# Kernel optimization log

Hardware: AMD Instinct MI355X
Metric: run time of the kernel (lower is better)

The kernel has to match this reference:

```python
import math
import jax, jax.numpy as jnp
import numpy as np

EMBED_SIZE = 1024
NUM_HEADS = 16
HEAD_DIM = EMBED_SIZE // NUM_HEADS
N, L = 8, 1024
MASK_FILL = -1e3  # value used by masked_fill in the original (NOT -inf)
SCALE = 1.0 / math.sqrt(EMBED_SIZE)  # original divides by embed_size**0.5, not head_dim


def setup_inputs() -> dict:
    key = jax.random.key(0)
    ks = jax.random.split(key, 7)
    values = jax.random.normal(ks[0], (N, L, EMBED_SIZE), dtype=jnp.float32)
    keys_t = jax.random.normal(ks[1], (N, L, EMBED_SIZE), dtype=jnp.float32)
    queries = jax.random.normal(ks[2], (N, L, EMBED_SIZE), dtype=jnp.float32)
    attn_mask = jax.random.randint(ks[3], (1, 1, L, L), 0, 2, dtype=jnp.int32)
    scr_key_padding_mask = jax.random.randint(ks[4], (N, 1, 1, L), 0, 2, dtype=jnp.int32)
    # fc_out: nn.Linear(embed_size, embed_size) with bias
    fc_w = jax.random.normal(ks[5], (EMBED_SIZE, EMBED_SIZE), dtype=jnp.float32) * (1.0 / math.sqrt(EMBED_SIZE))
    fc_b = jax.random.normal(ks[6], (EMBED_SIZE,), dtype=jnp.float32) * 0.01
    return {"values": values, "keys": keys_t, "queries": queries,
            "fc_w": fc_w, "fc_b": fc_b,
            "attn_mask": attn_mask, "scr_key_padding_mask": scr_key_padding_mask}


def reference(values, keys, queries, fc_w, fc_b, attn_mask, scr_key_padding_mask):
    n, q_len, e = queries.shape
    k_len = keys.shape[1]
    h, d = NUM_HEADS, HEAD_DIM
    # NOTE: the original defines per-head Linear projections but never applies them
    v = values.reshape(n, k_len, h, d)
    k = keys.reshape(n, k_len, h, d)
    q = queries.reshape(n, q_len, h, d)
    energy = jnp.einsum('nqhd,nkhd->nhqk', q, k)  # [n, h, q, k]
    am = attn_mask[:, :, :k_len, :k_len]
    energy = jnp.where(am == 0, MASK_FILL, energy)
    energy = jnp.where(scr_key_padding_mask == 0, MASK_FILL, energy)
    attention = jax.nn.softmax(energy * SCALE, axis=3)
    out = jnp.einsum('nhql,nlhd->nqhd', attention, v).reshape(n, q_len, h * d)
    return out @ fc_w.T + fc_b
```

## Files before the change

### kernel.cpp

```cpp
#include <hip/hip_runtime.h>

#define L_SEQ 1024
#define EMB 1024
#define NH 16
#define HD 64

typedef _Float16 half8 __attribute__((ext_vector_type(8)));
typedef _Float16 half4v __attribute__((ext_vector_type(4)));
typedef float f32x4 __attribute__((ext_vector_type(4)));
typedef float fvec4 __attribute__((ext_vector_type(4)));
typedef unsigned int u32;
typedef unsigned long long u64;

constexpr float C2 = 0.045084220027780106f;
constexpr float F2 = -45.08422002778011f;

constexpr int FP = 40;
constexpr int PP = 72;

__device__ __forceinline__ void async16(const void* g, void* l) {
    __builtin_amdgcn_global_load_lds((const __attribute__((address_space(1))) u32*)g,
                                     (__attribute__((address_space(3))) u32*)l, 16, 0, 0);
}

__global__ void pack_mask_kernel(const int* __restrict__ am, u32* __restrict__ bits) {
    const int i = blockIdx.x * 256 + threadIdx.x;
    const int lane = threadIdx.x & 63;
    u64 b = __ballot(am[i] != 0);
    if (lane == 0)       bits[i >> 5] = (u32)b;
    else if (lane == 32) bits[i >> 5] = (u32)(b >> 32);
}

__global__ void convert_w_kernel(const float* __restrict__ w, _Float16* __restrict__ o) {
    size_t i = ((size_t)blockIdx.x * blockDim.x + threadIdx.x) * 4;
    fvec4 v = *(const fvec4*)(w + i);
    half4v h;
#pragma unroll
    for (int j = 0; j < 4; ++j) h[j] = (_Float16)v[j];
    *(half4v*)(o + i) = h;
}

__global__ __launch_bounds__(256) void cvt_kv_kernel(
    const float* __restrict__ keys, const float* __restrict__ values,
    _Float16* __restrict__ K16, _Float16* __restrict__ Vt16)
{
    __shared__ __align__(16) _Float16 Vt[64 * PP];
    const int tid = threadIdx.x;
    const int kt = blockIdx.x, h = blockIdx.y, n = blockIdx.z;
    const int kbase = kt * 64;
    const int r = tid >> 2, c0 = (tid & 3) * 16;
    const int nh = n * NH + h;

    {
        const float* src = keys + ((size_t)(n * L_SEQ + kbase + r)) * EMB + h * HD + c0;
        fvec4 a0 = *(const fvec4*)(src),     a1 = *(const fvec4*)(src + 4);
        fvec4 a2 = *(const fvec4*)(src + 8), a3 = *(const fvec4*)(src + 12);
        half8 o0, o1;
#pragma unroll
        for (int j = 0; j < 4; ++j) {
            o0[j] = (_Float16)a0[j]; o0[j + 4] = (_Float16)a1[j];
            o1[j] = (_Float16)a2[j]; o1[j + 4] = (_Float16)a3[j];
        }
        _Float16* dst = K16 + ((size_t)nh * L_SEQ + kbase + r) * HD + c0;
        *(half8*)dst = o0; *(half8*)(dst + 8) = o1;
    }
    {
        const float* src = values + ((size_t)(n * L_SEQ + kbase + r)) * EMB + h * HD + c0;
        fvec4 vv[4];
        vv[0] = *(const fvec4*)(src);     vv[1] = *(const fvec4*)(src + 4);
        vv[2] = *(const fvec4*)(src + 8); vv[3] = *(const fvec4*)(src + 12);
#pragma unroll
        for (int i = 0; i < 16; ++i)
            Vt[(c0 + i) * PP + r] = (_Float16)vv[i >> 2][i & 3];
    }
    __syncthreads();
    {
        const int d = tid >> 2, k0 = (tid & 3) * 16;
        half8 v0 = *(const half8*)(&Vt[d * PP + k0]);
        half8 v1 = *(const half8*)(&Vt[d * PP + k0 + 8]);
        _Float16* dst = Vt16 + ((size_t)nh * HD + d) * L_SEQ + kbase + k0;
        *(half8*)dst = v0; *(half8*)(dst + 8) = v1;
    }
}

__global__ __launch_bounds__(256, 4) void attn_kernel(
    const _Float16* __restrict__ K16, const _Float16* __restrict__ Vt16,
    const float* __restrict__ queries, const u32* __restrict__ mbits,
    const int* __restrict__ pad_mask, _Float16* __restrict__ out_f16)
{
    __shared__ __align__(16) _Float16 K_lds[64 * 64];
    __shared__ __align__(16) _Float16 V_lds[64 * 64];
    __shared__ __align__(16) _Float16 P_lds[128 * PP];

    const int tid = threadIdx.x;
    const int lane = tid & 63;
    const int wave = tid >> 6;
    const int l16 = lane & 15;
    const int quad = lane >> 4;
    const int bid = blockIdx.x;
    const int nh = bid & 127, qt = bid >> 7;
    const int n = nh >> 4, h = nh & 15;
    const int qbase = qt * 128;
    const int xr = l16 & 7;

    half8 qf[2][2];
#pragma unroll
    for (int s = 0; s < 2; ++s) {
        const int qrow = qbase + wave * 32 + s * 16 + l16;
        const float* qp = queries + ((size_t)(n * L_SEQ + qrow)) * EMB + h * HD;
#pragma unroll
        for (int t = 0; t < 2; ++t) {
            fvec4 a = *(const fvec4*)(qp + t * 32 + quad * 8);
            fvec4 b = *(const fvec4*)(qp + t * 32 + quad * 8 + 4);
#pragma unroll
            for (int j = 0; j < 4; ++j) { qf[s][t][j] = (_Float16)a[j]; qf[s][t][j + 4] = (_Float16)b[j]; }
        }
    }

    f32x4 Ov[2][4];
#pragma unroll
    for (int s = 0; s < 2; ++s)
#pragma unroll
        for (int dt = 0; dt < 4; ++dt) Ov[s][dt] = (f32x4){0.f, 0.f, 0.f, 0.f};
    float lsum[2] = {0.f, 0.f};

    const _Float16* Kt_base = K16 + (size_t)nh * L_SEQ * HD;
    const _Float16* Vt_base = Vt16 + (size_t)nh * HD * L_SEQ;
    const int gch = (lane & 7) ^ ((lane >> 3) & 7);

    for (int kt = 0; kt < L_SEQ / 64; ++kt) {
        const int kbase = kt * 64;
        u32 w0[2], w1[2];
#pragma unroll
        for (int s = 0; s < 2; ++s) {
            const int qrow = qbase + wave * 32 + s * 16 + l16;
            w0[s] = mbits[qrow * 32 + kt * 2];
            w1[s] = mbits[qrow * 32 + kt * 2 + 1];
        }
        const u64 bal = __ballot(pad_mask[(size_t)n * L_SEQ + kbase + lane] != 0);
        const u32 plo = (u32)bal, phi = (u32)(bal >> 32);

        __syncthreads();
#pragma unroll
        for (int s2 = 0; s2 < 2; ++s2) {
            const int row = wave * 16 + s2 * 8 + (lane >> 3);
            async16(Kt_base + (size_t)(kbase + row) * HD + gch * 8, &K_lds[(wave * 16 + s2 * 8) * 64]);
            async16(Vt_base + (size_t)row * L_SEQ + kbase + gch * 8, &V_lds[(wave * 16 + s2 * 8) * 64]);
        }
        __syncthreads();

        f32x4 S[2][4];
#pragma unroll
        for (int s = 0; s < 2; ++s)
#pragma unroll
            for (int tj = 0; tj < 4; ++tj) S[s][tj] = (f32x4){0.f, 0.f, 0.f, 0.f};
#pragma unroll
        for (int tj = 0; tj < 4; ++tj) {
            const int krow = tj * 16 + l16;
            const _Float16* kr = &K_lds[krow * 64];
            const int c0 = (quad ^ xr) * 8;
            half8 k0 = *(const half8*)(kr + c0);
            half8 k1 = *(const half8*)(kr + (c0 ^ 32));
            S[0][tj] = __builtin_amdgcn_mfma_f32_16x16x32_f16(k0, qf[0][0], S[0][tj], 0, 0, 0);
            S[0][tj] = __builtin_amdgcn_mfma_f32_16x16x32_f16(k1, qf[0][1], S[0][tj], 0, 0, 0);
            S[1][tj] = __builtin_amdgcn_mfma_f32_16x16x32_f16(k0, qf[1][0], S[1][tj], 0, 0, 0);
            S[1][tj] = __builtin_amdgcn_mfma_f32_16x16x32_f16(k1, qf[1][1], S[1][tj], 0, 0, 0);
        }

#pragma unroll
        for (int s = 0; s < 2; ++s) {
            const u32 pw0 = w0[s] & plo, pw1 = w1[s] & phi;
#pragma unroll
            for (int tj = 0; tj < 4; ++tj) {
                const u32 m4 = ((tj & 2) ? pw1 : pw0) >> ((tj & 1) * 16 + quad * 4);
                float p[4];
#pragma unroll
                for (int reg = 0; reg < 4; ++reg) {
                    const float e = ((m4 >> reg) & 1u) ? S[s][tj][reg] * C2 : F2;
                    p[reg] = __builtin_amdgcn_exp2f(e);
                }
                lsum[s] += (p[0] + p[1]) + (p[2] + p[3]);
                half4v hp = {(_Float16)p[0], (_Float16)p[1], (_Float16)p[2], (_Float16)p[3]};
                *(half4v*)(&P_lds[(wave * 32 + s * 16 + l16) * PP + tj * 16 + quad * 4]) = hp;
            }
        }

        half8 pf0[2], pf1[2];
#pragma unroll
        for (int t = 0; t < 2; ++t) {
            pf0[t] = *(const half8*)(&P_lds[(wave * 32 + l16) * PP + t * 32 + quad * 8]);
            pf1[t] = *(const half8*)(&P_lds[(wave * 32 + 16 + l16) * PP + t * 32 + quad * 8]);
        }
#pragma unroll
        for (int t = 0; t < 2; ++t) {
            const int c0 = ((t * 4 + quad) ^ xr) * 8;
#pragma unroll
            for (int dt = 0; dt < 4; ++dt) {
                half8 vf = *(const half8*)(&V_lds[(dt * 16 + l16) * 64 + c0]);
                Ov[0][dt] = __builtin_amdgcn_mfma_f32_16x16x32_f16(pf0[t], vf, Ov[0][dt], 0, 0, 0);
                Ov[1][dt] = __builtin_amdgcn_mfma_f32_16x16x32_f16(pf1[t], vf, Ov[1][dt], 0, 0, 0);
            }
        }
    }

#pragma unroll
    for (int s = 0; s < 2; ++s) {
        lsum[s] += __shfl_xor(lsum[s], 16);
        lsum[s] += __shfl_xor(lsum[s], 32);
    }
#pragma unroll
    for (int s = 0; s < 2; ++s)
#pragma unroll
        for (int reg = 0; reg < 4; ++reg) {
            const float linv = 1.0f / __shfl(lsum[s], quad * 4 + reg);
            const int qrow = qbase + wave * 32 + s * 16 + quad * 4 + reg;
            _Float16* op = out_f16 + ((size_t)(n * L_SEQ + qrow)) * EMB + h * HD;
#pragma unroll
            for (int dt = 0; dt < 4; ++dt)
                op[dt * 16 + l16] = (_Float16)(Ov[s][dt][reg] * linv);
        }
}

__global__ __launch_bounds__(256) void fc_kernel(
    const _Float16* __restrict__ A, const _Float16* __restrict__ W,
    const float* __restrict__ bias, float* __restrict__ C)
{
    __shared__ __align__(16) _Float16 As[128 * FP];
    __shared__ __align__(16) _Float16 Ws[128 * FP];

    const int tid = threadIdx.x;
    const int lane = tid & 63;
    const int wv = tid >> 6;
    const int l16 = lane & 15;
    const int quad = lane >> 4;
    const int wm = (wv >> 1) * 64, wn = (wv & 1) * 64;
    const int Mb = blockIdx.x * 128, Nb = blockIdx.y * 128;

    f32x4 acc[4][4];
#pragma unroll
    for (int i = 0; i < 4; ++i)
#pragma unroll
        for (int j = 0; j < 4; ++j) acc[i][j] = (f32x4){0.f, 0.f, 0.f, 0.f};

    for (int k0 = 0; k0 < EMB; k0 += 32) {
        __syncthreads();
#pragma unroll
        for (int s = 0; s < 2; ++s) {
            const int id = tid + s * 256;
            const int row = id >> 2, ch = (id & 3) * 8;
            *(half8*)(&As[row * FP + ch]) = *(const half8*)(A + (size_t)(Mb + row) * EMB + k0 + ch);
            *(half8*)(&Ws[row * FP + ch]) = *(const half8*)(W + (size_t)(Nb + row) * EMB + k0 + ch);
        }
        __syncthreads();

        half8 af[4], bf[4];
#pragma unroll
        for (int i = 0; i < 4; ++i) {
            af[i] = *(const half8*)(&As[(wm + i * 16 + l16) * FP + quad * 8]);
            bf[i] = *(const half8*)(&Ws[(wn + i * 16 + l16) * FP + quad * 8]);
        }
#pragma unroll
        for (int i = 0; i < 4; ++i)
#pragma unroll
            for (int j = 0; j < 4; ++j)
                acc[i][j] = __builtin_amdgcn_mfma_f32_16x16x32_f16(af[i], bf[j], acc[i][j], 0, 0, 0);
    }

#pragma unroll
    for (int i = 0; i < 4; ++i) {
        const int m = Mb + wm + i * 16 + quad * 4;
#pragma unroll
        for (int j = 0; j < 4; ++j) {
            const int jc = Nb + wn + j * 16 + l16;
            const float b = bias[jc];
#pragma unroll
            for (int reg = 0; reg < 4; ++reg)
                C[(size_t)(m + reg) * EMB + jc] = acc[i][j][reg] + b;
        }
    }
}

extern "C" void kernel_launch(void* const* d_in, const int* in_sizes, int n_in,
                              void* d_out, int out_size, void* d_ws, size_t ws_size,
                              hipStream_t stream) {
    const float* values  = (const float*)d_in[0];
    const float* keys    = (const float*)d_in[1];
    const float* queries = (const float*)d_in[2];
    const float* fc_w    = (const float*)d_in[3];
    const float* fc_b    = (const float*)d_in[4];
    const int*   amask   = (const int*)d_in[5];
    const int*   pmask   = (const int*)d_in[6];
    float* out = (float*)d_out;

    char* w = (char*)d_ws;
    _Float16* attn_out = (_Float16*)w;
    _Float16* w_f16    = (_Float16*)(w + (size_t)16 * 1024 * 1024);
    u32*      mbits    = (u32*)(w + (size_t)18 * 1024 * 1024);
    _Float16* K16      = (_Float16*)(w + (size_t)19 * 1024 * 1024);
    _Float16* Vt16     = (_Float16*)(w + (size_t)35 * 1024 * 1024);

    pack_mask_kernel<<<4096, 256, 0, stream>>>(amask, mbits);
    convert_w_kernel<<<1024, 256, 0, stream>>>(fc_w, w_f16);
    cvt_kv_kernel<<<dim3(16, 16, 8), 256, 0, stream>>>(keys, values, K16, Vt16);
    attn_kernel<<<1024, 256, 0, stream>>>(K16, Vt16, queries, mbits, pmask, attn_out);
    fc_kernel<<<dim3(64, 8), 256, 0, stream>>>(attn_out, w_f16, fc_b, out);
}
```

Baseline: 239.6 us.

## Double-buffer K/V tiles, prepack pad mask, fold scale into K, mask via fp16 multiply

The attention loop now double-buffers the K and V tiles in LDS. The next tile's async loads are issued right after a single barrier per iteration, so the load-then-sync stall is gone. The padding mask is packed into bits by the existing mask kernel, which removes the per-iteration ballot over global ints. The softmax scale is folded into K during conversion. Masking now multiplies packed fp16 exponentials by a small LDS lookup table, and the row sum uses fdot2. Masked entries become exactly zero rather than exp(-45), and fully masked rows would give zeros instead of a uniform average. The doubled LDS and the occupancy hint lowered from 4 to 3 may reduce the number of resident blocks.

```diff
diff --git a/kernel.cpp b/kernel.cpp
--- a/kernel.cpp
+++ b/kernel.cpp
@@ -7,13 +7,13 @@
 
 typedef _Float16 half8 __attribute__((ext_vector_type(8)));
 typedef _Float16 half4v __attribute__((ext_vector_type(4)));
+typedef __fp16 h2 __attribute__((ext_vector_type(2)));
 typedef float f32x4 __attribute__((ext_vector_type(4)));
 typedef float fvec4 __attribute__((ext_vector_type(4)));
 typedef unsigned int u32;
 typedef unsigned long long u64;
 
 constexpr float C2 = 0.045084220027780106f;
-constexpr float F2 = -45.08422002778011f;
 
 constexpr int FP = 40;
 constexpr int PP = 72;
@@ -23,12 +23,19 @@
                                      (__attribute__((address_space(3))) u32*)l, 16, 0, 0);
 }
 
-__global__ void pack_mask_kernel(const int* __restrict__ am, u32* __restrict__ bits) {
+__global__ void pack_mask_kernel(const int* __restrict__ am, u32* __restrict__ bits,
+                                 const int* __restrict__ pad, u32* __restrict__ pbits) {
     const int i = blockIdx.x * 256 + threadIdx.x;
     const int lane = threadIdx.x & 63;
     u64 b = __ballot(am[i] != 0);
     if (lane == 0)       bits[i >> 5] = (u32)b;
     else if (lane == 32) bits[i >> 5] = (u32)(b >> 32);
+    if (blockIdx.x < 32) {
+        const int j = blockIdx.x * 256 + threadIdx.x;
+        u64 pb = __ballot(pad[j] != 0);
+        if (lane == 0)       pbits[j >> 5] = (u32)pb;
+        else if (lane == 32) pbits[j >> 5] = (u32)(pb >> 32);
+    }
 }
 
 __global__ void convert_w_kernel(const float* __restrict__ w, _Float16* __restrict__ o) {
@@ -58,8 +65,8 @@
         half8 o0, o1;
 #pragma unroll
         for (int j = 0; j < 4; ++j) {
-            o0[j] = (_Float16)a0[j]; o0[j + 4] = (_Float16)a1[j];
-            o1[j] = (_Float16)a2[j]; o1[j + 4] = (_Float16)a3[j];
+            o0[j] = (_Float16)(a0[j] * C2); o0[j + 4] = (_Float16)(a1[j] * C2);
+            o1[j] = (_Float16)(a2[j] * C2); o1[j + 4] = (_Float16)(a3[j] * C2);
         }
         _Float16* dst = K16 + ((size_t)nh * L_SEQ + kbase + r) * HD + c0;
         *(half8*)dst = o0; *(half8*)(dst + 8) = o1;
@@ -83,25 +90,50 @@
     }
 }
 
-__global__ __launch_bounds__(256, 4) void attn_kernel(
+__global__ __launch_bounds__(256, 3) void attn_kernel(
     const _Float16* __restrict__ K16, const _Float16* __restrict__ Vt16,
     const float* __restrict__ queries, const u32* __restrict__ mbits,
-    const int* __restrict__ pad_mask, _Float16* __restrict__ out_f16)
+    const u32* __restrict__ pbits, _Float16* __restrict__ out_f16)
 {
-    __shared__ __align__(16) _Float16 K_lds[64 * 64];
-    __shared__ __align__(16) _Float16 V_lds[64 * 64];
+    __shared__ __align__(16) _Float16 K_lds[2][64 * 64];
+    __shared__ __align__(16) _Float16 V_lds[2][64 * 64];
     __shared__ __align__(16) _Float16 P_lds[128 * PP];
-
-    const int tid = threadIdx.x;
+    __shared__ __align__(8)  u32 mtab[32];
+
+    const int tid  = threadIdx.x;
     const int lane = tid & 63;
     const int wave = tid >> 6;
-    const int l16 = lane & 15;
+    const int l16  = lane & 15;
     const int quad = lane >> 4;
-    const int bid = blockIdx.x;
+    const int bid  = blockIdx.x;
     const int nh = bid & 127, qt = bid >> 7;
     const int n = nh >> 4, h = nh & 15;
     const int qbase = qt * 128;
     const int xr = l16 & 7;
+    const int quad4 = quad * 4;
+
+    const _Float16* Kt_base = K16 + (size_t)nh * L_SEQ * HD;
+    const _Float16* Vt_base = Vt16 + (size_t)nh * HD * L_SEQ;
+    const int gch = (lane & 7) ^ ((lane >> 3) & 7);
+
+    auto stage = [&](int buf, int kt) {
+        const int kbase = kt * 64;
+#pragma unroll
+        for (int s2 = 0; s2 < 2; ++s2) {
+            const int row = wave * 16 + s2 * 8 + (lane >> 3);
+            async16(Kt_base + (size_t)(kbase + row) * HD + gch * 8,
+                    &K_lds[buf][(wave * 16 + s2 * 8) * 64]);
+            async16(Vt_base + (size_t)row * L_SEQ + kbase + gch * 8,
+                    &V_lds[buf][(wave * 16 + s2 * 8) * 64]);
+        }
+    };
+
+    stage(0, 0);
+
+    if (tid < 16) {
+        mtab[tid * 2]     = ((tid & 1) ? 0x3C00u : 0u) | ((tid & 2) ? 0x3C000000u : 0u);
+        mtab[tid * 2 + 1] = ((tid & 4) ? 0x3C00u : 0u) | ((tid & 8) ? 0x3C000000u : 0u);
+    }
 
     half8 qf[2][2];
 #pragma unroll
@@ -123,41 +155,33 @@
 #pragma unroll
         for (int dt = 0; dt < 4; ++dt) Ov[s][dt] = (f32x4){0.f, 0.f, 0.f, 0.f};
     float lsum[2] = {0.f, 0.f};
-
-    const _Float16* Kt_base = K16 + (size_t)nh * L_SEQ * HD;
-    const _Float16* Vt_base = Vt16 + (size_t)nh * HD * L_SEQ;
-    const int gch = (lane & 7) ^ ((lane >> 3) & 7);
-
+    const h2 one2 = {(__fp16)1.f, (__fp16)1.f};
+
+    int cur = 0;
+#pragma unroll 2
     for (int kt = 0; kt < L_SEQ / 64; ++kt) {
-        const int kbase = kt * 64;
-        u32 w0[2], w1[2];
+        __syncthreads();
+        if (kt + 1 < L_SEQ / 64) stage(cur ^ 1, kt + 1);
+
+        uint2 wm[2];
 #pragma unroll
         for (int s = 0; s < 2; ++s) {
             const int qrow = qbase + wave * 32 + s * 16 + l16;
-            w0[s] = mbits[qrow * 32 + kt * 2];
-            w1[s] = mbits[qrow * 32 + kt * 2 + 1];
-        }
-        const u64 bal = __ballot(pad_mask[(size_t)n * L_SEQ + kbase + lane] != 0);
-        const u32 plo = (u32)bal, phi = (u32)(bal >> 32);
-
-        __syncthreads();
-#pragma unroll
-        for (int s2 = 0; s2 < 2; ++s2) {
-            const int row = wave * 16 + s2 * 8 + (lane >> 3);
-            async16(Kt_base + (size_t)(kbase + row) * HD + gch * 8, &K_lds[(wave * 16 + s2 * 8) * 64]);
-            async16(Vt_base + (size_t)row * L_SEQ + kbase + gch * 8, &V_lds[(wave * 16 + s2 * 8) * 64]);
-        }
-        __syncthreads();
+            wm[s] = *(const uint2*)(&mbits[qrow * 32 + kt * 2]);
+        }
+        const u32 plo = pbits[(n << 5) + (kt << 1)];
+        const u32 phi = pbits[(n << 5) + (kt << 1) + 1];
 
         f32x4 S[2][4];
 #pragma unroll
         for (int s = 0; s < 2; ++s)
 #pragma unroll
             for (int tj = 0; tj < 4; ++tj) S[s][tj] = (f32x4){0.f, 0.f, 0.f, 0.f};
+
+        const _Float16* kb = &K_lds[cur][0];
 #pragma unroll
         for (int tj = 0; tj < 4; ++tj) {
-            const int krow = tj * 16 + l16;
-            const _Float16* kr = &K_lds[krow * 64];
+            const _Float16* kr = kb + (tj * 16 + l16) * 64;
             const int c0 = (quad ^ xr) * 8;
             half8 k0 = *(const half8*)(kr + c0);
             half8 k1 = *(const half8*)(kr + (c0 ^ 32));
@@ -169,22 +193,27 @@
 
 #pragma unroll
         for (int s = 0; s < 2; ++s) {
-            const u32 pw0 = w0[s] & plo, pw1 = w1[s] & phi;
+            const u32 pw0 = wm[s].x & plo, pw1 = wm[s].y & phi;
 #pragma unroll
             for (int tj = 0; tj < 4; ++tj) {
-                const u32 m4 = ((tj & 2) ? pw1 : pw0) >> ((tj & 1) * 16 + quad * 4);
-                float p[4];
-#pragma unroll
-                for (int reg = 0; reg < 4; ++reg) {
-                    const float e = ((m4 >> reg) & 1u) ? S[s][tj][reg] * C2 : F2;
-                    p[reg] = __builtin_amdgcn_exp2f(e);
-                }
-                lsum[s] += (p[0] + p[1]) + (p[2] + p[3]);
-                half4v hp = {(_Float16)p[0], (_Float16)p[1], (_Float16)p[2], (_Float16)p[3]};
-                *(half4v*)(&P_lds[(wave * 32 + s * 16 + l16) * PP + tj * 16 + quad * 4]) = hp;
+                const u32 m4 = (((tj & 2) ? pw1 : pw0) >> ((tj & 1) * 16 + quad4)) & 15u;
+                const uint2 mm = *(const uint2*)(&mtab[m4 * 2]);
+                const float p0 = __builtin_amdgcn_exp2f(S[s][tj][0]);
+                const float p1 = __builtin_amdgcn_exp2f(S[s][tj][1]);
+                const float p2 = __builtin_amdgcn_exp2f(S[s][tj][2]);
+                const float p3 = __builtin_amdgcn_exp2f(S[s][tj][3]);
+                const h2 q01 = __builtin_amdgcn_cvt_pkrtz(p0, p1) * __builtin_bit_cast(h2, mm.x);
+                const h2 q23 = __builtin_amdgcn_cvt_pkrtz(p2, p3) * __builtin_bit_cast(h2, mm.y);
+                lsum[s] = __builtin_amdgcn_fdot2(q01, one2, lsum[s], false);
+                lsum[s] = __builtin_amdgcn_fdot2(q23, one2, lsum[s], false);
+                uint2 st;
+                st.x = __builtin_bit_cast(u32, q01);
+                st.y = __builtin_bit_cast(u32, q23);
+                *(uint2*)(&P_lds[(wave * 32 + s * 16 + l16) * PP + tj * 16 + quad4]) = st;
             }
         }
 
+        const _Float16* vb = &V_lds[cur][0];
         half8 pf0[2], pf1[2];
 #pragma unroll
         for (int t = 0; t < 2; ++t) {
@@ -196,11 +225,12 @@
             const int c0 = ((t * 4 + quad) ^ xr) * 8;
 #pragma unroll
             for (int dt = 0; dt < 4; ++dt) {
-                half8 vf = *(const half8*)(&V_lds[(dt * 16 + l16) * 64 + c0]);
+                half8 vf = *(const half8*)(&vb[(dt * 16 + l16) * 64 + c0]);
                 Ov[0][dt] = __builtin_amdgcn_mfma_f32_16x16x32_f16(pf0[t], vf, Ov[0][dt], 0, 0, 0);
                 Ov[1][dt] = __builtin_amdgcn_mfma_f32_16x16x32_f16(pf1[t], vf, Ov[1][dt], 0, 0, 0);
             }
         }
+        cur ^= 1;
     }
 
 #pragma unroll
@@ -212,8 +242,8 @@
     for (int s = 0; s < 2; ++s)
 #pragma unroll
         for (int reg = 0; reg < 4; ++reg) {
-            const float linv = 1.0f / __shfl(lsum[s], quad * 4 + reg);
-            const int qrow = qbase + wave * 32 + s * 16 + quad * 4 + reg;
+            const float linv = 1.0f / fmaxf(__shfl(lsum[s], quad4 + reg), 1e-25f);
+            const int qrow = qbase + wave * 32 + s * 16 + quad4 + reg;
             _Float16* op = out_f16 + ((size_t)(n * L_SEQ + qrow)) * EMB + h * HD;
 #pragma unroll
             for (int dt = 0; dt < 4; ++dt)
@@ -296,12 +326,13 @@
     _Float16* attn_out = (_Float16*)w;
     _Float16* w_f16    = (_Float16*)(w + (size_t)16 * 1024 * 1024);
     u32*      mbits    = (u32*)(w + (size_t)18 * 1024 * 1024);
+    u32*      pbits    = (u32*)(w + (size_t)18 * 1024 * 1024 + 128 * 1024);
     _Float16* K16      = (_Float16*)(w + (size_t)19 * 1024 * 1024);
     _Float16* Vt16     = (_Float16*)(w + (size_t)35 * 1024 * 1024);
 
-    pack_mask_kernel<<<4096, 256, 0, stream>>>(amask, mbits);
+    pack_mask_kernel<<<4096, 256, 0, stream>>>(amask, mbits, pmask, pbits);
     convert_w_kernel<<<1024, 256, 0, stream>>>(fc_w, w_f16);
     cvt_kv_kernel<<<dim3(16, 16, 8), 256, 0, stream>>>(keys, values, K16, Vt16);
-    attn_kernel<<<1024, 256, 0, stream>>>(K16, Vt16, queries, mbits, pmask, attn_out);
+    attn_kernel<<<1024, 256, 0, stream>>>(K16, Vt16, queries, mbits, pbits, attn_out);
     fc_kernel<<<dim3(64, 8), 256, 0, stream>>>(attn_out, w_f16, fc_b, out);
 }
```

Result: no change. 235.7 us (-1.6%).
